# Performance work log

Measured on AMD Instinct MI355X. Metric: run time of the kernel, lower is better.

Reference implementation:

```python
import jax, jax.numpy as jnp
import numpy as np

B, S, D = 4, 2048, 1024
H = 16
HD = D // H  # 64

def setup_inputs() -> dict:
    key = jax.random.key(0)
    ks = jax.random.split(key, 7)
    s = 0.02
    return {
        "x": jax.random.normal(ks[0], (B, S, D), dtype=jnp.float32),
        "Wq": jax.random.normal(ks[1], (D, D), dtype=jnp.float32) * s,
        "bq": jax.random.normal(ks[2], (D,), dtype=jnp.float32) * s,
        "Wk": jax.random.normal(ks[3], (D, D), dtype=jnp.float32) * s,
        "bk": jax.random.normal(ks[4], (D,), dtype=jnp.float32) * s,
        "Wv": jax.random.normal(ks[5], (D, D), dtype=jnp.float32) * s,
        "bv": jax.random.normal(ks[6], (D,), dtype=jnp.float32) * s,
    }

def reference(x, Wq, bq, Wk, bk, Wv, bv):
    bs, seq, _ = x.shape
    q = (x @ Wq.T + bq).reshape(bs, seq, H, HD).transpose(0, 2, 1, 3)  # [b,h,s,d]
    k = (x @ Wk.T + bk).reshape(bs, seq, H, HD).transpose(0, 2, 1, 3)
    v = (x @ Wv.T + bv).reshape(bs, seq, H, HD).transpose(0, 2, 1, 3)
    scores = jnp.einsum('bhqd,bhkd->bhqk', q, k) / jnp.sqrt(jnp.float32(HD))
    probs = jax.nn.softmax(scores, axis=-1)  # dropout p=0 -> identity
    att = jnp.einsum('bhqk,bhkd->bhqd', probs, v)
    return att.transpose(0, 2, 1, 3).reshape(bs, seq, H * HD)
```

## Files before the change

### kernel.cpp

```cpp
#include <hip/hip_runtime.h>

typedef __bf16 bf16x8 __attribute__((ext_vector_type(8)));
typedef float f32x4 __attribute__((ext_vector_type(4)));

#define BATCH 4
#define SEQ   2048
#define DIM   1024
#define NH    16
#define HD    64
#define ECF   0.18033688f

__device__ __forceinline__ unsigned short f2bf(float f) {
  union { float f; unsigned u; } v; v.f = f;
  unsigned u = v.u;
  u += 0x7FFF + ((u >> 16) & 1);
  return (unsigned short)(u >> 16);
}

__device__ __forceinline__ void g2lds16(const unsigned short* g, unsigned short* l) {
  __builtin_amdgcn_global_load_lds(
      (const __attribute__((address_space(1))) unsigned int*)g,
      (__attribute__((address_space(3))) unsigned int*)l, 16, 0, 0);
}

__global__ __launch_bounds__(256) void cast_all_kernel(
    const float* __restrict__ x,  const float* __restrict__ Wq,
    const float* __restrict__ Wk, const float* __restrict__ Wv,
    unsigned short* __restrict__ xb,  unsigned short* __restrict__ wqb,
    unsigned short* __restrict__ wkb, unsigned short* __restrict__ wvb) {
  const int XG = (BATCH * SEQ * DIM) / 8;
  const int WG = (DIM * DIM) / 8;
  int i = blockIdx.x * 256 + threadIdx.x;
  const float* in; unsigned short* out; float sc = 1.0f; int off;
  if (i < XG)               { in = x;  out = xb;  off = i; }
  else if (i < XG + WG)     { in = Wq; out = wqb; off = i - XG; sc = ECF; }
  else if (i < XG + 2 * WG) { in = Wk; out = wkb; off = i - XG - WG; }
  else                      { in = Wv; out = wvb; off = i - XG - 2 * WG; }
  const float4* p = (const float4*)in + (size_t)off * 2;
  float4 a = p[0], b = p[1];
  unsigned short r[8];
  r[0] = f2bf(a.x * sc); r[1] = f2bf(a.y * sc); r[2] = f2bf(a.z * sc); r[3] = f2bf(a.w * sc);
  r[4] = f2bf(b.x * sc); r[5] = f2bf(b.y * sc); r[6] = f2bf(b.z * sc); r[7] = f2bf(b.w * sc);
  *(uint4*)&out[(size_t)off * 8] = *(uint4*)r;
}

__global__ __launch_bounds__(256) void gemm_qkv(
    const unsigned short* __restrict__ A,
    const unsigned short* __restrict__ Wqp, const unsigned short* __restrict__ Wkp,
    const unsigned short* __restrict__ Wvp,
    const float* __restrict__ bqp, const float* __restrict__ bkp,
    const float* __restrict__ bvp,
    unsigned short* __restrict__ oq, unsigned short* __restrict__ ok,
    unsigned short* __restrict__ ov) {
  __shared__ unsigned short As[128 * 32];
  __shared__ unsigned short Bs[128 * 32];
  const int z = blockIdx.z;
  const unsigned short* W = (z == 0) ? Wqp : (z == 1) ? Wkp : Wvp;
  const float* bias        = (z == 0) ? bqp : (z == 1) ? bkp : bvp;
  unsigned short* outp     = (z == 0) ? oq  : (z == 1) ? ok  : ov;
  const float bsc          = (z == 0) ? ECF : 1.0f;
  const int mode = (z == 2) ? 1 : 0;

  const int tid  = threadIdx.x;
  const int wave = tid >> 6;
  const int lane = tid & 63;
  const int lm   = lane & 15;
  const int qd   = lane >> 4;
  const int m0 = blockIdx.x * 128;
  const int n0 = blockIdx.y * 128;
  const int wm = (wave >> 1) * 64;
  const int wn = (wave & 1) * 64;

  const f32x4 zero = {0.f, 0.f, 0.f, 0.f};
  f32x4 acc[4][4];
#pragma unroll
  for (int i = 0; i < 4; ++i)
#pragma unroll
    for (int j = 0; j < 4; ++j) acc[i][j] = zero;

  const int srow = tid >> 2;
  const int scol = (((tid & 3) ^ ((tid >> 3) & 3))) * 8;
  const int cs   = (qd ^ ((lm >> 1) & 3)) * 8;

  for (int kt = 0; kt < DIM; kt += 32) {
    __syncthreads();
    g2lds16(&A[(size_t)(m0 + srow) * DIM + kt + scol],       &As[(size_t)tid * 8]);
    g2lds16(&A[(size_t)(m0 + 64 + srow) * DIM + kt + scol],  &As[2048 + (size_t)tid * 8]);
    g2lds16(&W[(size_t)(n0 + srow) * DIM + kt + scol],       &Bs[(size_t)tid * 8]);
    g2lds16(&W[(size_t)(n0 + 64 + srow) * DIM + kt + scol],  &Bs[2048 + (size_t)tid * 8]);
    __syncthreads();

    bf16x8 af[4], bfr[4];
#pragma unroll
    for (int i = 0; i < 4; ++i) af[i]  = *(const bf16x8*)&As[(wm + i * 16 + lm) * 32 + cs];
#pragma unroll
    for (int j = 0; j < 4; ++j) bfr[j] = *(const bf16x8*)&Bs[(wn + j * 16 + lm) * 32 + cs];
#pragma unroll
    for (int i = 0; i < 4; ++i)
#pragma unroll
      for (int j = 0; j < 4; ++j)
        acc[i][j] = __builtin_amdgcn_mfma_f32_16x16x32_bf16(af[i], bfr[j], acc[i][j], 0, 0, 0);
  }

#pragma unroll
  for (int j = 0; j < 4; ++j) {
    int col = n0 + wn + j * 16 + lm;
    float bb = bias[col] * bsc;
    int h = col >> 6, hd = col & 63;
#pragma unroll
    for (int i = 0; i < 4; ++i) {
      int rowb = m0 + wm + i * 16 + qd * 4;
      int b = rowb >> 11, s = rowb & 2047;
      if (mode == 0) {
#pragma unroll
        for (int r = 0; r < 4; ++r) {
          float v = acc[i][j][r] + bb;
          outp[((size_t)(b * NH + h) * SEQ + (s + r)) * HD + hd] = f2bf(v);
        }
      } else {
        unsigned short pk[4];
#pragma unroll
        for (int r = 0; r < 4; ++r) pk[r] = f2bf(acc[i][j][r] + bb);
        size_t idx = ((size_t)(b * NH + h) * HD + hd) * SEQ + s;
        *(uint2*)&outp[idx] = *(uint2*)pk;
      }
    }
  }
}

__global__ __launch_bounds__(128, 2) void flash_kernel(
    const unsigned short* __restrict__ Qw, const unsigned short* __restrict__ Kw,
    const unsigned short* __restrict__ Vw, float* __restrict__ out) {
  __shared__ unsigned short Ks2[2 * 64 * 32];
  __shared__ unsigned short Vs2[2 * 64 * 32];
  __shared__ unsigned short Ps[128 * 64];
  __shared__ float Ls[128];

  const int tid  = threadIdx.x;
  const int w    = tid >> 6;
  const int lane = tid & 63;
  const int lm   = lane & 15;
  const int qd   = lane >> 4;
  const int bh   = blockIdx.y;
  const int q0   = blockIdx.x * 128;

  const unsigned short* Qbase = Qw + (size_t)bh * (SEQ * HD);
  const unsigned short* Kbase = Kw + (size_t)bh * (SEQ * HD);
  const unsigned short* Vbase = Vw + (size_t)bh * (HD * SEQ);

  bf16x8 qf[4][2];
#pragma unroll
  for (int g = 0; g < 4; ++g)
#pragma unroll
    for (int h = 0; h < 2; ++h)
      qf[g][h] = *(const bf16x8*)&Qbase[(size_t)(q0 + w * 64 + g * 16 + lm) * HD + h * 32 + qd * 8];

  const f32x4 zero = {0.f, 0.f, 0.f, 0.f};
  f32x4 o[4][4];
#pragma unroll
  for (int g = 0; g < 4; ++g)
#pragma unroll
    for (int jn = 0; jn < 4; ++jn) o[g][jn] = zero;
  float psg[4] = {0.f, 0.f, 0.f, 0.f};

  const int c0 = tid, c1 = tid + 128;
  const int r0 = c0 >> 2, p0s = ((c0 & 3) ^ ((c0 >> 3) & 3)) * 8;
  const int r1 = c1 >> 2, p1s = ((c1 & 3) ^ ((c1 >> 3) & 3)) * 8;

  const int cs  = (qd ^ ((lm >> 1) & 3)) * 8;
  const int pk_key = lm & 7;

  for (int kt = 0; kt < SEQ / 64; ++kt) {
    const int k0 = kt * 64;
    __syncthreads();
    g2lds16(&Kbase[(size_t)(k0 + r0) * HD + p0s],      &Ks2[(size_t)c0 * 8]);
    g2lds16(&Kbase[(size_t)(k0 + r1) * HD + p1s],      &Ks2[(size_t)c1 * 8]);
    g2lds16(&Kbase[(size_t)(k0 + r0) * HD + 32 + p0s], &Ks2[2048 + (size_t)c0 * 8]);
    g2lds16(&Kbase[(size_t)(k0 + r1) * HD + 32 + p1s], &Ks2[2048 + (size_t)c1 * 8]);
    g2lds16(&Vbase[(size_t)r0 * SEQ + k0 + p0s],       &Vs2[(size_t)c0 * 8]);
    g2lds16(&Vbase[(size_t)r1 * SEQ + k0 + p1s],       &Vs2[(size_t)c1 * 8]);
    g2lds16(&Vbase[(size_t)r0 * SEQ + k0 + 32 + p0s],  &Vs2[2048 + (size_t)c0 * 8]);
    g2lds16(&Vbase[(size_t)r1 * SEQ + k0 + 32 + p1s],  &Vs2[2048 + (size_t)c1 * 8]);
    __syncthreads();

#pragma unroll
    for (int jk = 0; jk < 4; ++jk) {
      bf16x8 kf0 = *(const bf16x8*)&Ks2[(jk * 16 + lm) * 32 + cs];
      bf16x8 kf1 = *(const bf16x8*)&Ks2[2048 + (jk * 16 + lm) * 32 + cs];
      f32x4 st[4];
#pragma unroll
      for (int g = 0; g < 4; ++g) {
        st[g] = __builtin_amdgcn_mfma_f32_16x16x32_bf16(kf0, qf[g][0], zero, 0, 0, 0);
        st[g] = __builtin_amdgcn_mfma_f32_16x16x32_bf16(kf1, qf[g][1], st[g], 0, 0, 0);
      }
#pragma unroll
      for (int g = 0; g < 4; ++g) {
        float p0 = __builtin_amdgcn_exp2f(st[g][0]);
        float p1 = __builtin_amdgcn_exp2f(st[g][1]);
        float p2 = __builtin_amdgcn_exp2f(st[g][2]);
        float p3 = __builtin_amdgcn_exp2f(st[g][3]);
        psg[g] += (p0 + p1) + (p2 + p3);
        uint2 pk;
        pk.x = __builtin_amdgcn_perm(__float_as_uint(p1), __float_as_uint(p0), 0x07060302);
        pk.y = __builtin_amdgcn_perm(__float_as_uint(p3), __float_as_uint(p2), 0x07060302);
        int sw = (2 * jk + (qd >> 1)) ^ pk_key;
        *(uint2*)&Ps[(w * 64 + g * 16 + lm) * 64 + sw * 8 + (qd & 1) * 4] = pk;
      }
    }

    asm volatile("s_waitcnt lgkmcnt(0)" ::: "memory");

#pragma unroll
    for (int h2 = 0; h2 < 2; ++h2) {
      bf16x8 pf[4];
#pragma unroll
      for (int g = 0; g < 4; ++g) {
        int sw = (h2 * 4 + qd) ^ pk_key;
        pf[g] = *(const bf16x8*)&Ps[(w * 64 + g * 16 + lm) * 64 + sw * 8];
      }
#pragma unroll
      for (int jn = 0; jn < 4; ++jn) {
        bf16x8 vf = *(const bf16x8*)&Vs2[h2 * 2048 + (jn * 16 + lm) * 32 + cs];
#pragma unroll
        for (int g = 0; g < 4; ++g)
          o[g][jn] = __builtin_amdgcn_mfma_f32_16x16x32_bf16(pf[g], vf, o[g][jn], 0, 0, 0);
      }
    }
  }

#pragma unroll
  for (int g = 0; g < 4; ++g) {
    float l = psg[g];
    l += __shfl_xor(l, 16); l += __shfl_xor(l, 32);
    if (qd == 0) Ls[w * 64 + g * 16 + lm] = l;
  }
  asm volatile("s_waitcnt lgkmcnt(0)" ::: "memory");

  const int b = bh >> 4, hh = bh & 15;
#pragma unroll
  for (int g = 0; g < 4; ++g)
#pragma unroll
    for (int r = 0; r < 4; ++r) {
      float inv = 1.0f / Ls[w * 64 + g * 16 + qd * 4 + r];
      int qrow = q0 + w * 64 + g * 16 + qd * 4 + r;
#pragma unroll
      for (int jn = 0; jn < 4; ++jn)
        out[(size_t)(b * SEQ + qrow) * DIM + hh * HD + jn * 16 + lm] = o[g][jn][r] * inv;
    }
}

extern "C" void kernel_launch(void* const* d_in, const int* in_sizes, int n_in,
                              void* d_out, int out_size, void* d_ws, size_t ws_size,
                              hipStream_t stream) {
  const float* x  = (const float*)d_in[0];
  const float* Wq = (const float*)d_in[1];
  const float* bq = (const float*)d_in[2];
  const float* Wk = (const float*)d_in[3];
  const float* bk = (const float*)d_in[4];
  const float* Wv = (const float*)d_in[5];
  const float* bv = (const float*)d_in[6];
  float* out = (float*)d_out;

  unsigned short* ws = (unsigned short*)d_ws;
  const size_t XE = (size_t)BATCH * SEQ * DIM;
  const size_t WE = (size_t)DIM * DIM;
  unsigned short* xb  = ws;
  unsigned short* wqb = xb + XE;
  unsigned short* wkb = wqb + WE;
  unsigned short* wvb = wkb + WE;
  unsigned short* qb  = wvb + WE;
  unsigned short* kb  = qb + XE;
  unsigned short* vb  = kb + XE;

  const int total_groups = (int)(XE / 8 + 3 * (WE / 8));
  cast_all_kernel<<<total_groups / 256, 256, 0, stream>>>(
      x, Wq, Wk, Wv, xb, wqb, wkb, wvb);

  dim3 gg(64, 8, 3);
  gemm_qkv<<<gg, 256, 0, stream>>>(xb, wqb, wkb, wvb, bq, bk, bv, qb, kb, vb);

  dim3 fg(SEQ / 128, BATCH * NH);
  flash_kernel<<<fg, 128, 0, stream>>>(qb, kb, vb, out);
}
```

Before: 249.3 us.

## Rewrite flash kernel with 32x32 MFMA, register-resident P, double-buffered K/V

The attention kernel moves from 16x16x32 to 32x32x16 bf16 MFMAs. It keeps the softmax probabilities in registers, using v_permlane32_swap to rearrange them into A-operand layout, which removes the Ps shared-memory round trip. K/V tiles are now double-buffered, so the next tile's global-to-LDS load overlaps with compute and one barrier per iteration goes away. Blocks grow to 256 threads covering 256 queries each. The larger accumulators raise register pressure and may lower occupancy.

Measured after the change: 248.6 us. Within noise of the previous version (-0.3%).

```diff
diff --git a/kernel.cpp b/kernel.cpp
--- a/kernel.cpp
+++ b/kernel.cpp
@@ -2,6 +2,7 @@
 
 typedef __bf16 bf16x8 __attribute__((ext_vector_type(8)));
 typedef float f32x4 __attribute__((ext_vector_type(4)));
+typedef float f32x16 __attribute__((ext_vector_type(16)));
 
 #define BATCH 4
 #define SEQ   2048
@@ -21,6 +22,13 @@
   __builtin_amdgcn_global_load_lds(
       (const __attribute__((address_space(1))) unsigned int*)g,
       (__attribute__((address_space(3))) unsigned int*)l, 16, 0, 0);
+}
+
+__device__ __forceinline__ unsigned packbf(float a, float b) {
+  __bf16 lo = (__bf16)a, hi = (__bf16)b;
+  unsigned short ul = __builtin_bit_cast(unsigned short, lo);
+  unsigned short uh = __builtin_bit_cast(unsigned short, hi);
+  return (unsigned)ul | ((unsigned)uh << 16);
 }
 
 __global__ __launch_bounds__(256) void cast_all_kernel(
@@ -128,124 +136,130 @@
   }
 }
 
-__global__ __launch_bounds__(128, 2) void flash_kernel(
-    const unsigned short* __restrict__ Qw, const unsigned short* __restrict__ Kw,
-    const unsigned short* __restrict__ Vw, float* __restrict__ out) {
-  __shared__ unsigned short Ks2[2 * 64 * 32];
-  __shared__ unsigned short Vs2[2 * 64 * 32];
-  __shared__ unsigned short Ps[128 * 64];
-  __shared__ float Ls[128];
+__global__ __launch_bounds__(256, 2) void flash_kernel(
+    const unsigned short* __restrict__ Qp, const unsigned short* __restrict__ Kp,
+    const unsigned short* __restrict__ Vp, float* __restrict__ out) {
+  __shared__ __align__(16) unsigned short Ks[2][64 * 64];
+  __shared__ __align__(16) unsigned short Vs[2][64 * 64];
+  __shared__ float Ls[4][2][32];
 
   const int tid  = threadIdx.x;
   const int w    = tid >> 6;
   const int lane = tid & 63;
-  const int lm   = lane & 15;
-  const int qd   = lane >> 4;
+  const int l31  = lane & 31;
+  const int hi   = lane >> 5;
   const int bh   = blockIdx.y;
-  const int q0   = blockIdx.x * 128;
-
-  const unsigned short* Qbase = Qw + (size_t)bh * (SEQ * HD);
-  const unsigned short* Kbase = Kw + (size_t)bh * (SEQ * HD);
-  const unsigned short* Vbase = Vw + (size_t)bh * (HD * SEQ);
-
-  bf16x8 qf[4][2];
-#pragma unroll
-  for (int g = 0; g < 4; ++g)
-#pragma unroll
-    for (int h = 0; h < 2; ++h)
-      qf[g][h] = *(const bf16x8*)&Qbase[(size_t)(q0 + w * 64 + g * 16 + lm) * HD + h * 32 + qd * 8];
-
-  const f32x4 zero = {0.f, 0.f, 0.f, 0.f};
-  f32x4 o[4][4];
-#pragma unroll
-  for (int g = 0; g < 4; ++g)
-#pragma unroll
-    for (int jn = 0; jn < 4; ++jn) o[g][jn] = zero;
-  float psg[4] = {0.f, 0.f, 0.f, 0.f};
-
-  const int c0 = tid, c1 = tid + 128;
-  const int r0 = c0 >> 2, p0s = ((c0 & 3) ^ ((c0 >> 3) & 3)) * 8;
-  const int r1 = c1 >> 2, p1s = ((c1 & 3) ^ ((c1 >> 3) & 3)) * 8;
-
-  const int cs  = (qd ^ ((lm >> 1) & 3)) * 8;
-  const int pk_key = lm & 7;
-
+  const int wq0  = blockIdx.x * 256 + w * 64;
+
+  const unsigned short* Qb = Qp + (size_t)bh * (SEQ * HD);
+  const unsigned short* Kb = Kp + (size_t)bh * (SEQ * HD);
+  const unsigned short* Vb = Vp + (size_t)bh * (HD * SEQ);
+
+  bf16x8 qf[2][4];
+#pragma unroll
+  for (int qb = 0; qb < 2; ++qb)
+#pragma unroll
+    for (int db = 0; db < 4; ++db)
+      qf[qb][db] = *(const bf16x8*)&Qb[(size_t)(wq0 + qb * 32 + l31) * HD + db * 16 + hi * 8];
+
+  f32x16 o[2][2];
+#pragma unroll
+  for (int qb = 0; qb < 2; ++qb)
+#pragma unroll
+    for (int jn = 0; jn < 2; ++jn)
+#pragma unroll
+      for (int r = 0; r < 16; ++r) o[qb][jn][r] = 0.f;
+  float psum[2] = {0.f, 0.f};
+
+  const int c0 = tid, c1 = tid + 256;
+  const int kr0 = c0 >> 3, kp0 = ((c0 & 7) ^ (kr0 & 7)) * 8;
+  const int kr1 = c1 >> 3, kp1 = ((c1 & 7) ^ (kr1 & 7)) * 8;
+  const int r7 = l31 & 7;
+
+  auto STAGE = [&](int buf, int k0) {
+    g2lds16(&Kb[(size_t)(k0 + kr0) * HD + kp0], &Ks[buf][c0 * 8]);
+    g2lds16(&Kb[(size_t)(k0 + kr1) * HD + kp1], &Ks[buf][c1 * 8]);
+    g2lds16(&Vb[(size_t)kr0 * SEQ + k0 + kp0],  &Vs[buf][c0 * 8]);
+    g2lds16(&Vb[(size_t)kr1 * SEQ + k0 + kp1],  &Vs[buf][c1 * 8]);
+  };
+
+  STAGE(0, 0);
+  int cur = 0;
   for (int kt = 0; kt < SEQ / 64; ++kt) {
-    const int k0 = kt * 64;
     __syncthreads();
-    g2lds16(&Kbase[(size_t)(k0 + r0) * HD + p0s],      &Ks2[(size_t)c0 * 8]);
-    g2lds16(&Kbase[(size_t)(k0 + r1) * HD + p1s],      &Ks2[(size_t)c1 * 8]);
-    g2lds16(&Kbase[(size_t)(k0 + r0) * HD + 32 + p0s], &Ks2[2048 + (size_t)c0 * 8]);
-    g2lds16(&Kbase[(size_t)(k0 + r1) * HD + 32 + p1s], &Ks2[2048 + (size_t)c1 * 8]);
-    g2lds16(&Vbase[(size_t)r0 * SEQ + k0 + p0s],       &Vs2[(size_t)c0 * 8]);
-    g2lds16(&Vbase[(size_t)r1 * SEQ + k0 + p1s],       &Vs2[(size_t)c1 * 8]);
-    g2lds16(&Vbase[(size_t)r0 * SEQ + k0 + 32 + p0s],  &Vs2[2048 + (size_t)c0 * 8]);
-    g2lds16(&Vbase[(size_t)r1 * SEQ + k0 + 32 + p1s],  &Vs2[2048 + (size_t)c1 * 8]);
-    __syncthreads();
-
-#pragma unroll
-    for (int jk = 0; jk < 4; ++jk) {
-      bf16x8 kf0 = *(const bf16x8*)&Ks2[(jk * 16 + lm) * 32 + cs];
-      bf16x8 kf1 = *(const bf16x8*)&Ks2[2048 + (jk * 16 + lm) * 32 + cs];
-      f32x4 st[4];
-#pragma unroll
-      for (int g = 0; g < 4; ++g) {
-        st[g] = __builtin_amdgcn_mfma_f32_16x16x32_bf16(kf0, qf[g][0], zero, 0, 0, 0);
-        st[g] = __builtin_amdgcn_mfma_f32_16x16x32_bf16(kf1, qf[g][1], st[g], 0, 0, 0);
-      }
-#pragma unroll
-      for (int g = 0; g < 4; ++g) {
-        float p0 = __builtin_amdgcn_exp2f(st[g][0]);
-        float p1 = __builtin_amdgcn_exp2f(st[g][1]);
-        float p2 = __builtin_amdgcn_exp2f(st[g][2]);
-        float p3 = __builtin_amdgcn_exp2f(st[g][3]);
-        psg[g] += (p0 + p1) + (p2 + p3);
-        uint2 pk;
-        pk.x = __builtin_amdgcn_perm(__float_as_uint(p1), __float_as_uint(p0), 0x07060302);
-        pk.y = __builtin_amdgcn_perm(__float_as_uint(p3), __float_as_uint(p2), 0x07060302);
-        int sw = (2 * jk + (qd >> 1)) ^ pk_key;
-        *(uint2*)&Ps[(w * 64 + g * 16 + lm) * 64 + sw * 8 + (qd & 1) * 4] = pk;
-      }
-    }
-
-    asm volatile("s_waitcnt lgkmcnt(0)" ::: "memory");
-
-#pragma unroll
-    for (int h2 = 0; h2 < 2; ++h2) {
-      bf16x8 pf[4];
-#pragma unroll
-      for (int g = 0; g < 4; ++g) {
-        int sw = (h2 * 4 + qd) ^ pk_key;
-        pf[g] = *(const bf16x8*)&Ps[(w * 64 + g * 16 + lm) * 64 + sw * 8];
-      }
-#pragma unroll
-      for (int jn = 0; jn < 4; ++jn) {
-        bf16x8 vf = *(const bf16x8*)&Vs2[h2 * 2048 + (jn * 16 + lm) * 32 + cs];
-#pragma unroll
-        for (int g = 0; g < 4; ++g)
-          o[g][jn] = __builtin_amdgcn_mfma_f32_16x16x32_bf16(pf[g], vf, o[g][jn], 0, 0, 0);
-      }
-    }
-  }
-
-#pragma unroll
-  for (int g = 0; g < 4; ++g) {
-    float l = psg[g];
-    l += __shfl_xor(l, 16); l += __shfl_xor(l, 32);
-    if (qd == 0) Ls[w * 64 + g * 16 + lm] = l;
+    if (kt + 1 < SEQ / 64) STAGE(cur ^ 1, (kt + 1) * 64);
+
+    const unsigned short* Kc = &Ks[cur][0];
+    const unsigned short* Vc = &Vs[cur][0];
+
+    bf16x8 pa[2][4];
+#pragma unroll
+    for (int kb = 0; kb < 2; ++kb) {
+      f32x16 s0 = {0,0,0,0,0,0,0,0,0,0,0,0,0,0,0,0};
+      f32x16 s1 = {0,0,0,0,0,0,0,0,0,0,0,0,0,0,0,0};
+#pragma unroll
+      for (int db = 0; db < 4; ++db) {
+        int ch = (db * 2 + hi) ^ r7;
+        bf16x8 kf = *(const bf16x8*)&Kc[((kb * 32 + l31) * 8 + ch) * 8];
+        s0 = __builtin_amdgcn_mfma_f32_32x32x16_bf16(kf, qf[0][db], s0, 0, 0, 0);
+        s1 = __builtin_amdgcn_mfma_f32_32x32x16_bf16(kf, qf[1][db], s1, 0, 0, 0);
+      }
+#pragma unroll
+      for (int qb = 0; qb < 2; ++qb) {
+        const f32x16 s = qb ? s1 : s0;
+        float p[16];
+#pragma unroll
+        for (int r = 0; r < 16; ++r) p[r] = __builtin_amdgcn_exp2f(s[r]);
+        psum[qb] += ((p[0] + p[1]) + (p[2] + p[3])) + ((p[4] + p[5]) + (p[6] + p[7]))
+                  + ((p[8] + p[9]) + (p[10] + p[11])) + ((p[12] + p[13]) + (p[14] + p[15]));
+        unsigned w01 = packbf(p[0],  p[1]),  w23 = packbf(p[2],  p[3]);
+        unsigned w45 = packbf(p[4],  p[5]),  w67 = packbf(p[6],  p[7]);
+        unsigned w89 = packbf(p[8],  p[9]),  wab = packbf(p[10], p[11]);
+        unsigned wcd = packbf(p[12], p[13]), wef = packbf(p[14], p[15]);
+        asm volatile("v_permlane32_swap_b32 %0, %1" : "+v"(w01), "+v"(w45));
+        asm volatile("v_permlane32_swap_b32 %0, %1" : "+v"(w23), "+v"(w67));
+        asm volatile("v_permlane32_swap_b32 %0, %1" : "+v"(w89), "+v"(wcd));
+        asm volatile("v_permlane32_swap_b32 %0, %1" : "+v"(wab), "+v"(wef));
+        union { unsigned u[4]; bf16x8 v; } flo, fhi;
+        flo.u[0] = w01; flo.u[1] = w23; flo.u[2] = w45; flo.u[3] = w67;
+        fhi.u[0] = w89; fhi.u[1] = wab; fhi.u[2] = wcd; fhi.u[3] = wef;
+        pa[qb][kb * 2]     = flo.v;
+        pa[qb][kb * 2 + 1] = fhi.v;
+      }
+    }
+
+#pragma unroll
+    for (int ks = 0; ks < 4; ++ks) {
+#pragma unroll
+      for (int jn = 0; jn < 2; ++jn) {
+        int row = jn * 32 + l31;
+        int ch = (ks * 2 + hi) ^ r7;
+        bf16x8 vf = *(const bf16x8*)&Vc[(row * 8 + ch) * 8];
+        o[0][jn] = __builtin_amdgcn_mfma_f32_32x32x16_bf16(pa[0][ks], vf, o[0][jn], 0, 0, 0);
+        o[1][jn] = __builtin_amdgcn_mfma_f32_32x32x16_bf16(pa[1][ks], vf, o[1][jn], 0, 0, 0);
+      }
+    }
+    cur ^= 1;
+  }
+
+#pragma unroll
+  for (int qb = 0; qb < 2; ++qb) {
+    float l = psum[qb] + __shfl_xor(psum[qb], 32);
+    if (hi == 0) Ls[w][qb][l31] = 1.0f / l;
   }
   asm volatile("s_waitcnt lgkmcnt(0)" ::: "memory");
 
   const int b = bh >> 4, hh = bh & 15;
 #pragma unroll
-  for (int g = 0; g < 4; ++g)
-#pragma unroll
-    for (int r = 0; r < 4; ++r) {
-      float inv = 1.0f / Ls[w * 64 + g * 16 + qd * 4 + r];
-      int qrow = q0 + w * 64 + g * 16 + qd * 4 + r;
-#pragma unroll
-      for (int jn = 0; jn < 4; ++jn)
-        out[(size_t)(b * SEQ + qrow) * DIM + hh * HD + jn * 16 + lm] = o[g][jn][r] * inv;
+  for (int qb = 0; qb < 2; ++qb)
+#pragma unroll
+    for (int r = 0; r < 16; ++r) {
+      int crow = (r & 3) + 8 * (r >> 2) + 4 * hi;
+      float inv = Ls[w][qb][crow];
+      int qrow = wq0 + qb * 32 + crow;
+      float* po = &out[(size_t)(b * SEQ + qrow) * DIM + hh * HD + l31];
+      po[0]  = o[qb][0][r] * inv;
+      po[32] = o[qb][1][r] * inv;
     }
 }
 
@@ -279,6 +293,6 @@
   dim3 gg(64, 8, 3);
   gemm_qkv<<<gg, 256, 0, stream>>>(xb, wqb, wkb, wvb, bq, bk, bv, qb, kb, vb);
 
-  dim3 fg(SEQ / 128, BATCH * NH);
-  flash_kernel<<<fg, 128, 0, stream>>>(qb, kb, vb, out);
-}
+  dim3 fg(SEQ / 256, BATCH * NH);
+  flash_kernel<<<fg, 256, 0, stream>>>(qb, kb, vb, out);
+}
```

## Pipeline QKV GEMM with triple-buffered LDS and larger 256x128 tiles

Applied to the files above, without the earlier changes.

Rewrites the QKV projection GEMM main loop to use a three-stage LDS ring buffer with 64-wide K tiles. Global-to-LDS loads for stage t+2 are issued while MFMAs run on stage t, synchronised with explicit vmcnt waits and raw s_barrier. Block size grows to 512 threads covering a 256x128 tile, and setprio raises the MFMA phase's priority. This targets exposed load latency and the two full barriers per small K-step, at the cost of more LDS per block (one block per CU) and more fragile hand-written synchronisation.

Measured after the change: 242.6 us. 2.7% less time.

```diff
diff --git a/kernel.cpp b/kernel.cpp
--- a/kernel.cpp
+++ b/kernel.cpp
@@ -44,7 +44,7 @@
   *(uint4*)&out[(size_t)off * 8] = *(uint4*)r;
 }
 
-__global__ __launch_bounds__(256) void gemm_qkv(
+__global__ __launch_bounds__(512, 1) void gemm_qkv(
     const unsigned short* __restrict__ A,
     const unsigned short* __restrict__ Wqp, const unsigned short* __restrict__ Wkp,
     const unsigned short* __restrict__ Wvp,
@@ -52,8 +52,8 @@
     const float* __restrict__ bvp,
     unsigned short* __restrict__ oq, unsigned short* __restrict__ ok,
     unsigned short* __restrict__ ov) {
-  __shared__ unsigned short As[128 * 32];
-  __shared__ unsigned short Bs[128 * 32];
+  __shared__ __align__(16) unsigned short sm[3 * 24576];
+
   const int z = blockIdx.z;
   const unsigned short* W = (z == 0) ? Wqp : (z == 1) ? Wkp : Wvp;
   const float* bias        = (z == 0) ? bqp : (z == 1) ? bkp : bvp;
@@ -62,14 +62,14 @@
   const int mode = (z == 2) ? 1 : 0;
 
   const int tid  = threadIdx.x;
-  const int wave = tid >> 6;
+  const int w    = tid >> 6;
   const int lane = tid & 63;
   const int lm   = lane & 15;
   const int qd   = lane >> 4;
-  const int m0 = blockIdx.x * 128;
+  const int m0 = blockIdx.x * 256;
   const int n0 = blockIdx.y * 128;
-  const int wm = (wave >> 1) * 64;
-  const int wn = (wave & 1) * 64;
+  const int wm = (w & 3) * 64;
+  const int wn = (w >> 2) * 64;
 
   const f32x4 zero = {0.f, 0.f, 0.f, 0.f};
   f32x4 acc[4][4];
@@ -78,29 +78,74 @@
 #pragma unroll
     for (int j = 0; j < 4; ++j) acc[i][j] = zero;
 
-  const int srow = tid >> 2;
-  const int scol = (((tid & 3) ^ ((tid >> 3) & 3))) * 8;
-  const int cs   = (qd ^ ((lm >> 1) & 3)) * 8;
-
-  for (int kt = 0; kt < DIM; kt += 32) {
-    __syncthreads();
-    g2lds16(&A[(size_t)(m0 + srow) * DIM + kt + scol],       &As[(size_t)tid * 8]);
-    g2lds16(&A[(size_t)(m0 + 64 + srow) * DIM + kt + scol],  &As[2048 + (size_t)tid * 8]);
-    g2lds16(&W[(size_t)(n0 + srow) * DIM + kt + scol],       &Bs[(size_t)tid * 8]);
-    g2lds16(&W[(size_t)(n0 + 64 + srow) * DIM + kt + scol],  &Bs[2048 + (size_t)tid * 8]);
-    __syncthreads();
-
-    bf16x8 af[4], bfr[4];
-#pragma unroll
-    for (int i = 0; i < 4; ++i) af[i]  = *(const bf16x8*)&As[(wm + i * 16 + lm) * 32 + cs];
-#pragma unroll
-    for (int j = 0; j < 4; ++j) bfr[j] = *(const bf16x8*)&Bs[(wn + j * 16 + lm) * 32 + cs];
-#pragma unroll
-    for (int i = 0; i < 4; ++i)
+  const int r0 = tid >> 3;
+  const int sp = ((tid & 7) ^ (r0 & 7)) * 8;
+
+#define SA(buf, t4, i) g2lds16(&A[(size_t)(m0 + r0 + 64*(i)) * DIM + (t4)*64 + sp], \
+                               &sm[(buf)*24576 + (r0 + 64*(i))*64 + (tid & 7)*8])
+#define SB(buf, t4, i) g2lds16(&W[(size_t)(n0 + r0 + 64*(i)) * DIM + (t4)*64 + sp], \
+                               &sm[(buf)*24576 + 16384 + (r0 + 64*(i))*64 + (tid & 7)*8])
+#define BARR() asm volatile("s_barrier" ::: "memory")
+
+  const int rk = lm & 7;
+
+  SA(0, 0, 0); SA(0, 0, 1); SA(0, 0, 2); SA(0, 0, 3); SB(0, 0, 0); SB(0, 0, 1);
+  SA(1, 1, 0); SA(1, 1, 1); SA(1, 1, 2); SA(1, 1, 3); SB(1, 1, 0); SB(1, 1, 1);
+  asm volatile("s_waitcnt vmcnt(6)" ::: "memory");
+  BARR();
+
+  for (int t = 0; t < DIM / 64; ++t) {
+    const int cur = t % 3;
+    const int nb  = (t + 2) % 3;
+    const bool st = (t + 2) < DIM / 64;
+    const unsigned short* Ab = &sm[cur * 24576];
+    const unsigned short* Bb = &sm[cur * 24576 + 16384];
+
+    {
+      bf16x8 af[4], bfr[4];
+#pragma unroll
+      for (int i = 0; i < 4; ++i)
+        af[i]  = *(const bf16x8*)&Ab[(wm + i * 16 + lm) * 64 + ((qd ^ rk) * 8)];
 #pragma unroll
       for (int j = 0; j < 4; ++j)
-        acc[i][j] = __builtin_amdgcn_mfma_f32_16x16x32_bf16(af[i], bfr[j], acc[i][j], 0, 0, 0);
+        bfr[j] = *(const bf16x8*)&Bb[(wn + j * 16 + lm) * 64 + ((qd ^ rk) * 8)];
+      if (st) { SA(nb, t + 2, 0); SA(nb, t + 2, 1); SA(nb, t + 2, 2); }
+      BARR();
+      __builtin_amdgcn_s_setprio(1);
+#pragma unroll
+      for (int i = 0; i < 4; ++i)
+#pragma unroll
+        for (int j = 0; j < 4; ++j)
+          acc[i][j] = __builtin_amdgcn_mfma_f32_16x16x32_bf16(af[i], bfr[j], acc[i][j], 0, 0, 0);
+      __builtin_amdgcn_s_setprio(0);
+      BARR();
+    }
+
+    {
+      bf16x8 af[4], bfr[4];
+#pragma unroll
+      for (int i = 0; i < 4; ++i)
+        af[i]  = *(const bf16x8*)&Ab[(wm + i * 16 + lm) * 64 + (((4 + qd) ^ rk) * 8)];
+#pragma unroll
+      for (int j = 0; j < 4; ++j)
+        bfr[j] = *(const bf16x8*)&Bb[(wn + j * 16 + lm) * 64 + (((4 + qd) ^ rk) * 8)];
+      if (st) { SA(nb, t + 2, 3); SB(nb, t + 2, 0); SB(nb, t + 2, 1); }
+      BARR();
+      __builtin_amdgcn_s_setprio(1);
+#pragma unroll
+      for (int i = 0; i < 4; ++i)
+#pragma unroll
+        for (int j = 0; j < 4; ++j)
+          acc[i][j] = __builtin_amdgcn_mfma_f32_16x16x32_bf16(af[i], bfr[j], acc[i][j], 0, 0, 0);
+      __builtin_amdgcn_s_setprio(0);
+      if (st) asm volatile("s_waitcnt vmcnt(6)" ::: "memory");
+      else    asm volatile("s_waitcnt vmcnt(0)" ::: "memory");
+      BARR();
+    }
   }
+#undef SA
+#undef SB
+#undef BARR
 
 #pragma unroll
   for (int j = 0; j < 4; ++j) {
@@ -276,8 +321,8 @@
   cast_all_kernel<<<total_groups / 256, 256, 0, stream>>>(
       x, Wq, Wk, Wv, xb, wqb, wkb, wvb);
 
-  dim3 gg(64, 8, 3);
-  gemm_qkv<<<gg, 256, 0, stream>>>(xb, wqb, wkb, wvb, bq, bk, bv, qb, kb, vb);
+  dim3 gg(32, 8, 3);
+  gemm_qkv<<<gg, 512, 0, stream>>>(xb, wqb, wkb, wvb, bq, bk, bv, qb, kb, vb);
 
   dim3 fg(SEQ / 128, BATCH * NH);
   flash_kernel<<<fg, 128, 0, stream>>>(qb, kb, vb, out);
```
